# Kernel tuning notes

Measured on AMD Instinct MI355X. Metric: run time of the kernel, lower is better.

The kernel has to match this reference:

```python
import jax, jax.numpy as jnp
import numpy as np

B, N, D, H = 1, 512, 128, 128  # batch, seq, pair dim, hidden dim
EPS = 1e-6  # flax nnx LayerNorm default epsilon


def _layernorm(x, scale, bias):
    m = jnp.mean(x, axis=-1, keepdims=True)
    v = jnp.var(x, axis=-1, keepdims=True)
    return (x - m) * jax.lax.rsqrt(v + EPS) * scale + bias


def setup_inputs() -> dict:
    key = jax.random.key(0)
    ks = jax.random.split(key, 12)
    s = 0.02  # param init scale
    inp = {
        "x": jax.random.normal(ks[0], (B, N, N, D), jnp.float32),
        "src_mask": jnp.ones((B, N), jnp.float32),
        # first LayerNorm
        "ln1_scale": jnp.ones((D,), jnp.float32),
        "ln1_bias": jnp.zeros((D,), jnp.float32),
        # left/right projections
        "wl": jax.random.normal(ks[1], (D, H), jnp.float32) * s,
        "bl": jnp.zeros((H,), jnp.float32),
        "wr": jax.random.normal(ks[2], (D, H), jnp.float32) * s,
        "br": jnp.zeros((H,), jnp.float32),
        # gates (original inits kernel=0, bias=1; use small random kernels + bias=1 for a nontrivial baseline)
        "wlg": jax.random.normal(ks[3], (D, H), jnp.float32) * s,
        "blg": jnp.ones((H,), jnp.float32),
        "wrg": jax.random.normal(ks[4], (D, H), jnp.float32) * s,
        "brg": jnp.ones((H,), jnp.float32),
        "wog": jax.random.normal(ks[5], (D, H), jnp.float32) * s,
        "bog": jnp.ones((H,), jnp.float32),
        # output LayerNorm + projection
        "ln2_scale": jnp.ones((H,), jnp.float32),
        "ln2_bias": jnp.zeros((H,), jnp.float32),
        "wo": jax.random.normal(ks[6], (H, D), jnp.float32) * s,
        "bo": jnp.zeros((D,), jnp.float32),
    }
    return inp


def reference(x, src_mask, ln1_scale, ln1_bias, wl, bl, wr, br, wlg, blg,
              wrg, brg, wog, bog, ln2_scale, ln2_bias, wo, bo):
    # mask[b,i,j] = src_mask[b,i] * src_mask[b,j]  -> [B,N,N,1]
    sm = src_mask.astype(jnp.float32)
    mask = (sm[:, :, None] * sm[:, None, :])[..., None]

    xn = _layernorm(x, ln1_scale, ln1_bias)  # [B,N,N,D]

    # projections, mask, gates (gating after transpose in the original is
    # elementwise, hence equivalent applied pre-transpose)
    left = (xn @ wl + bl) * mask * jax.nn.sigmoid(xn @ wlg + blg)   # [B,N,N,H]
    right = (xn @ wr + br) * mask * jax.nn.sigmoid(xn @ wrg + brg)  # [B,N,N,H]
    out_gate = jax.nn.sigmoid(xn @ wog + bog)                       # [B,N,N,H]

    # 'ingoing' mix: out[b,i,j,d] = sum_k left[b,k,i,d] * right[b,k,j,d]
    out = jnp.einsum('bkid,bkjd->bijd', left, right)

    out = _layernorm(out, ln2_scale, ln2_bias) * out_gate
    return out @ wo + bo
```

## Files before the change

kernel.cpp:

```cpp
#include <hip/hip_runtime.h>
#include <hip/hip_bf16.h>


#define NSEQ 512
#define NN 262144
#define PL 262400
#define DMODEL 128

typedef __attribute__((ext_vector_type(8))) short short8;
typedef __attribute__((ext_vector_type(4))) float f32x4;

__device__ __forceinline__ unsigned short f2b(float f) {
    __hip_bfloat16 h = __float2bfloat16(f);
    return *reinterpret_cast<unsigned short*>(&h);
}
__device__ __forceinline__ float b2f(unsigned short u) {
    __hip_bfloat16 h;
    *reinterpret_cast<unsigned short*>(&h) = u;
    return __bfloat162float(h);
}
__device__ __forceinline__ unsigned int cvt_pk_bf16(float lo, float hi) {
    unsigned int r;
    asm("v_cvt_pk_bf16_f32 %0, %1, %2" : "=v"(r) : "v"(lo), "v"(hi));
    return r;
}
__device__ __forceinline__ float sigfast(float x) {
    return __builtin_amdgcn_rcpf(1.f + __builtin_amdgcn_exp2f(x * -1.44269504f));
}

__global__ __launch_bounds__(256) void k_wt_all(
    const float* __restrict__ w0, const float* __restrict__ w1,
    const float* __restrict__ w2, const float* __restrict__ w3,
    const float* __restrict__ w4, const float* __restrict__ w5,
    unsigned short* __restrict__ wt) {
    int bid = blockIdx.x;
    int mat = bid >> 6;
    const float* w = (mat == 0) ? w0 : (mat == 1) ? w1 : (mat == 2) ? w2
                   : (mat == 3) ? w3 : (mat == 4) ? w4 : w5;
    int idx = (bid & 63) * 256 + threadIdx.x;
    int d = idx >> 7, h = idx & 127;
    wt[mat * 16384 + h * 128 + d] = f2b(w[idx]);
}

__global__ __launch_bounds__(256) void k_ln1(const float* __restrict__ x,
                                             const float* __restrict__ sc,
                                             const float* __restrict__ bi,
                                             unsigned short* __restrict__ xn) {
    int t = threadIdx.x;
    int l = t & 31;
    size_t row = (size_t)blockIdx.x * 8 + (t >> 5);
    float4 v = *(const float4*)(x + row * DMODEL + l * 4);
    float s  = v.x + v.y + v.z + v.w;
    float sq = v.x * v.x + v.y * v.y + v.z * v.z + v.w * v.w;
    #pragma unroll
    for (int m = 1; m < 32; m <<= 1) {
        s  += __shfl_xor(s, m);
        sq += __shfl_xor(sq, m);
    }
    float mean = s * (1.f / 128.f);
    float var  = sq * (1.f / 128.f) - mean * mean;
    float inv  = rsqrtf(var + 1e-6f);
    float4 scv = *(const float4*)(sc + l * 4);
    float4 biv = *(const float4*)(bi + l * 4);
    uint2 pk;
    pk.x = cvt_pk_bf16((v.x - mean) * inv * scv.x + biv.x,
                       (v.y - mean) * inv * scv.y + biv.y);
    pk.y = cvt_pk_bf16((v.z - mean) * inv * scv.z + biv.z,
                       (v.w - mean) * inv * scv.w + biv.w);
    *(uint2*)(xn + row * DMODEL + l * 4) = pk;
}

__global__ __launch_bounds__(256, 2) void k_proj(
    const unsigned short* __restrict__ xn,
    const float* __restrict__ src_mask,
    const unsigned short* __restrict__ wt,
    const float* __restrict__ bl,  const float* __restrict__ blg,
    const float* __restrict__ br,  const float* __restrict__ brg,
    const float* __restrict__ bog,
    unsigned short* __restrict__ left_t,
    unsigned short* __restrict__ right_t,
    unsigned short* __restrict__ og) {
    __shared__ __align__(16) unsigned short As[64 * 136];
    const int t = threadIdx.x;
    const int lane = t & 63;
    const int wv = t >> 6;
    const int a0 = blockIdx.x * 64;
    const int b  = blockIdx.y;
    const int n0 = wv * 32;

    short8 bfA[2][4], bfB[2][4];
    auto loadB = [&](short8 (&dst)[2][4], int mat) {
        const unsigned short* base = wt + mat * 16384 + (lane >> 4) * 8;
        #pragma unroll
        for (int nf = 0; nf < 2; ++nf)
            #pragma unroll
            for (int kc = 0; kc < 4; ++kc)
                dst[nf][kc] = *(const short8*)(
                    base + (n0 + nf * 16 + (lane & 15)) * 128 + kc * 32);
    };
    loadB(bfA, 0);
    loadB(bfB, 1);

    #pragma unroll
    for (int it = 0; it < 4; ++it) {
        int idx = it * 256 + t;
        int row = idx >> 4, c = idx & 15;
        *(short8*)(&As[row * 136 + c * 8]) =
            *(const short8*)(xn + ((size_t)(a0 + row) * NSEQ + b) * DMODEL + c * 8);
    }
    __syncthreads();

    short8 af[4][4];
    #pragma unroll
    for (int mf = 0; mf < 4; ++mf)
        #pragma unroll
        for (int kc = 0; kc < 4; ++kc)
            af[mf][kc] = *(const short8*)(
                &As[(mf * 16 + (lane & 15)) * 136 + kc * 32 + (lane >> 4) * 8]);

    f32x4 acc0[4][2], acc1[4][2];
    float smb = src_mask[b];

    auto mmat = [&](f32x4 (&acc)[4][2], short8 (&bf)[2][4]) {
        #pragma unroll
        for (int mf = 0; mf < 4; ++mf)
            #pragma unroll
            for (int nf = 0; nf < 2; ++nf)
                acc[mf][nf] = f32x4{0.f, 0.f, 0.f, 0.f};
        #pragma unroll
        for (int kc = 0; kc < 4; ++kc)
            #pragma unroll
            for (int mf = 0; mf < 4; ++mf)
                #pragma unroll
                for (int nf = 0; nf < 2; ++nf)
                    acc[mf][nf] = __builtin_amdgcn_mfma_f32_16x16x32_bf16(
                        af[mf][kc], bf[nf][kc], acc[mf][nf], 0, 0, 0);
    };
    auto epi_pair = [&](const float* b1, const float* b2, unsigned short* dst) {
        float mkv[16];
        #pragma unroll
        for (int mf = 0; mf < 4; ++mf)
            #pragma unroll
            for (int j = 0; j < 4; ++j)
                mkv[mf * 4 + j] =
                    src_mask[a0 + mf * 16 + ((lane >> 4) << 2) + j] * smb;
        #pragma unroll
        for (int nf = 0; nf < 2; ++nf) {
            int h = n0 + nf * 16 + (lane & 15);
            float b1v = b1[h], b2v = b2[h];
            #pragma unroll
            for (int mf = 0; mf < 4; ++mf) {
                int abase = a0 + mf * 16 + ((lane >> 4) << 2);
                float o_[4];
                #pragma unroll
                for (int j = 0; j < 4; ++j) {
                    float pv = acc0[mf][nf][j] + b1v;
                    float gv = acc1[mf][nf][j] + b2v;
                    o_[j] = pv * mkv[mf * 4 + j] * sigfast(gv);
                }
                uint2 pk;
                pk.x = cvt_pk_bf16(o_[0], o_[1]);
                pk.y = cvt_pk_bf16(o_[2], o_[3]);
                *(uint2*)(dst + (size_t)h * PL + (size_t)b * NSEQ + abase) = pk;
            }
        }
    };

    mmat(acc0, bfA);
    loadB(bfA, 2);
    mmat(acc1, bfB);
    loadB(bfB, 3);
    epi_pair(bl, blg, left_t);
    mmat(acc0, bfA);
    loadB(bfA, 4);
    mmat(acc1, bfB);
    epi_pair(br, brg, right_t);
    mmat(acc0, bfA);

    __syncthreads();
    #pragma unroll
    for (int nf = 0; nf < 2; ++nf) {
        int h = n0 + nf * 16 + (lane & 15);
        float bv = bog[h];
        #pragma unroll
        for (int mf = 0; mf < 4; ++mf) {
            int rloc = mf * 16 + ((lane >> 4) << 2);
            #pragma unroll
            for (int j = 0; j < 4; ++j)
                As[(rloc + j) * 136 + h] = f2b(sigfast(acc0[mf][nf][j] + bv));
        }
    }
    __syncthreads();
    #pragma unroll
    for (int it = 0; it < 4; ++it) {
        int idx = it * 256 + t;
        int row = idx >> 4, c = idx & 15;
        *(short8*)(og + ((size_t)(a0 + row) * NSEQ + b) * DMODEL + c * 8) =
            *(const short8*)(&As[row * 136 + c * 8]);
    }
}

__global__ __launch_bounds__(256) void k_einsum(
    const unsigned short* __restrict__ lt,
    const unsigned short* __restrict__ rt,
    unsigned short* __restrict__ mid) {
    __shared__ __align__(16) unsigned short As[2][128 * 36];
    __shared__ __align__(16) unsigned short Bs[2][128 * 36];
    const int t = threadIdx.x, lane = t & 63, wv = t >> 6;
    const int bid = blockIdx.x;
    const int xcd = bid & 7, slot = bid >> 3;
    const int d = xcd * 16 + (slot >> 4);
    const int tile = slot & 15;
    const int i0 = (tile >> 2) * 128, j0 = (tile & 3) * 128;
    const int m0 = (wv >> 1) * 64, n0 = (wv & 1) * 64;
    const unsigned short* Ag = lt + (size_t)d * PL;
    const unsigned short* Bg = rt + (size_t)d * PL;

    const int row0 = t >> 2, sub0 = t & 3;
    const int row1 = (256 + t) >> 2, sub1 = t & 3;

    short8 ra[2], rb[2];
    auto loadTile = [&](int k0) {
        ra[0] = *(const short8*)(Ag + (size_t)(i0 + row0) * NSEQ + k0 + sub0 * 8);
        rb[0] = *(const short8*)(Bg + (size_t)(j0 + row0) * NSEQ + k0 + sub0 * 8);
        ra[1] = *(const short8*)(Ag + (size_t)(i0 + row1) * NSEQ + k0 + sub1 * 8);
        rb[1] = *(const short8*)(Bg + (size_t)(j0 + row1) * NSEQ + k0 + sub1 * 8);
    };
    auto writeTile = [&](int buf) {
        *(short8*)(&As[buf][row0 * 36 + sub0 * 8]) = ra[0];
        *(short8*)(&Bs[buf][row0 * 36 + sub0 * 8]) = rb[0];
        *(short8*)(&As[buf][row1 * 36 + sub1 * 8]) = ra[1];
        *(short8*)(&Bs[buf][row1 * 36 + sub1 * 8]) = rb[1];
    };

    f32x4 acc[4][4];
    #pragma unroll
    for (int mf = 0; mf < 4; ++mf)
        #pragma unroll
        for (int nf = 0; nf < 4; ++nf)
            acc[mf][nf] = f32x4{0.f, 0.f, 0.f, 0.f};

    loadTile(0);
    writeTile(0);
    int cur = 0;
    const int ko = (lane >> 4) * 8;
    for (int it = 0; it < 16; ++it) {
        __syncthreads();
        if (it < 15) loadTile((it + 1) * 32);
        short8 af[4], bf[4];
        #pragma unroll
        for (int mf = 0; mf < 4; ++mf)
            af[mf] = *(const short8*)(&As[cur][(m0 + mf * 16 + (lane & 15)) * 36 + ko]);
        #pragma unroll
        for (int nf = 0; nf < 4; ++nf)
            bf[nf] = *(const short8*)(&Bs[cur][(n0 + nf * 16 + (lane & 15)) * 36 + ko]);
        #pragma unroll
        for (int mf = 0; mf < 4; ++mf)
            #pragma unroll
            for (int nf = 0; nf < 4; ++nf)
                acc[mf][nf] = __builtin_amdgcn_mfma_f32_16x16x32_bf16(
                    af[mf], bf[nf], acc[mf][nf], 0, 0, 0);
        if (it < 15) writeTile(cur ^ 1);
        cur ^= 1;
    }
    unsigned short* out = mid + (size_t)d * PL;
    #pragma unroll
    for (int mf = 0; mf < 4; ++mf) {
        int rbase = i0 + m0 + mf * 16 + ((lane >> 4) << 2);
        #pragma unroll
        for (int nf = 0; nf < 4; ++nf) {
            int col = j0 + n0 + nf * 16 + (lane & 15);
            #pragma unroll
            for (int j = 0; j < 4; ++j)
                out[(size_t)(rbase + j) * NSEQ + col] = f2b(acc[mf][nf][j]);
        }
    }
}

__global__ __launch_bounds__(128) void k_ln2gate(
    const unsigned short* __restrict__ mid,
    const unsigned short* __restrict__ og,
    const float* __restrict__ sc, const float* __restrict__ bi,
    unsigned short* __restrict__ g) {
    __shared__ __align__(16) unsigned short lo[128 * 136];
    const int t = threadIdx.x;
    const size_t p0 = (size_t)blockIdx.x * 128;
    const size_t p = p0 + t;

    unsigned int vals[64];
    float s = 0.f, sq = 0.f;
    #pragma unroll
    for (int d2 = 0; d2 < 64; ++d2) {
        unsigned int a = mid[(size_t)(2 * d2)     * PL + p];
        unsigned int c = mid[(size_t)(2 * d2 + 1) * PL + p];
        vals[d2] = a | (c << 16);
        float fa = b2f((unsigned short)a), fc = b2f((unsigned short)c);
        s += fa + fc; sq += fa * fa + fc * fc;
    }
    float mean = s * (1.f / 128.f);
    float var  = sq * (1.f / 128.f) - mean * mean;
    float inv  = rsqrtf(var + 1e-6f);
    #pragma unroll
    for (int c = 0; c < 16; ++c) {
        short8 ov = *(const short8*)(og + p * DMODEL + c * 8);
        float y[8];
        #pragma unroll
        for (int e = 0; e < 8; ++e) {
            int d = c * 8 + e;
            unsigned int w = vals[d >> 1];
            float v = b2f((unsigned short)((d & 1) ? (w >> 16) : (w & 0xffff)));
            y[e] = ((v - mean) * inv * sc[d] + bi[d]) * b2f((unsigned short)ov[e]);
        }
        uint4 pk;
        pk.x = cvt_pk_bf16(y[0], y[1]);
        pk.y = cvt_pk_bf16(y[2], y[3]);
        pk.z = cvt_pk_bf16(y[4], y[5]);
        pk.w = cvt_pk_bf16(y[6], y[7]);
        *(uint4*)(&lo[t * 136 + c * 8]) = pk;
    }
    __syncthreads();
    #pragma unroll
    for (int i = 0; i < 16; ++i) {
        int idx = i * 128 + t;
        int row = idx >> 4, ch = idx & 15;
        *(short8*)(g + (p0 + row) * DMODEL + ch * 8) =
            *(const short8*)(&lo[row * 136 + ch * 8]);
    }
}

__global__ __launch_bounds__(256) void k_out(
    const unsigned short* __restrict__ g,
    const unsigned short* __restrict__ wt_o,
    const float* __restrict__ bo,
    float* __restrict__ out) {
    __shared__ __align__(16) unsigned short As[64 * 136];
    __shared__ __align__(16) unsigned short Bs[128 * 136];
    const int t = threadIdx.x, lane = t & 63, wv = t >> 6;
    const size_t r0 = (size_t)blockIdx.x * 64;
    const int n0 = wv * 32;
    for (int it = 0; it < 4; ++it) {
        int idx = it * 256 + t;
        int row = idx >> 4, c = idx & 15;
        *(short8*)(&As[row * 136 + c * 8]) =
            *(const short8*)(g + (r0 + row) * DMODEL + c * 8);
    }
    for (int it = 0; it < 8; ++it) {
        int idx = it * 256 + t;
        int h = idx >> 4, c = idx & 15;
        *(short8*)(&Bs[h * 136 + c * 8]) = *(const short8*)(wt_o + h * 128 + c * 8);
    }
    __syncthreads();
    f32x4 acc[4][2];
    #pragma unroll
    for (int mf = 0; mf < 4; ++mf)
        #pragma unroll
        for (int nf = 0; nf < 2; ++nf)
            acc[mf][nf] = f32x4{0.f, 0.f, 0.f, 0.f};
    #pragma unroll
    for (int kc = 0; kc < 4; ++kc) {
        int ko = kc * 32 + (lane >> 4) * 8;
        short8 af[4], bf[2];
        #pragma unroll
        for (int mf = 0; mf < 4; ++mf)
            af[mf] = *(const short8*)(&As[(mf * 16 + (lane & 15)) * 136 + ko]);
        #pragma unroll
        for (int nf = 0; nf < 2; ++nf)
            bf[nf] = *(const short8*)(&Bs[(n0 + nf * 16 + (lane & 15)) * 136 + ko]);
        #pragma unroll
        for (int mf = 0; mf < 4; ++mf)
            #pragma unroll
            for (int nf = 0; nf < 2; ++nf)
                acc[mf][nf] = __builtin_amdgcn_mfma_f32_16x16x32_bf16(
                    af[mf], bf[nf], acc[mf][nf], 0, 0, 0);
    }
    #pragma unroll
    for (int nf = 0; nf < 2; ++nf) {
        int n = n0 + nf * 16 + (lane & 15);
        float bv = bo[n];
        #pragma unroll
        for (int mf = 0; mf < 4; ++mf) {
            int rb = mf * 16 + ((lane >> 4) << 2);
            #pragma unroll
            for (int j = 0; j < 4; ++j)
                out[(r0 + rb + j) * DMODEL + n] = acc[mf][nf][j] + bv;
        }
    }
}

extern "C" void kernel_launch(void* const* d_in, const int* in_sizes, int n_in,
                              void* d_out, int out_size, void* d_ws, size_t ws_size,
                              hipStream_t stream) {
    const float* x    = (const float*)d_in[0];
    const float* sm   = (const float*)d_in[1];
    const float* ln1s = (const float*)d_in[2];
    const float* ln1b = (const float*)d_in[3];
    const float* wl   = (const float*)d_in[4];
    const float* bl   = (const float*)d_in[5];
    const float* wr   = (const float*)d_in[6];
    const float* br   = (const float*)d_in[7];
    const float* wlg  = (const float*)d_in[8];
    const float* blg  = (const float*)d_in[9];
    const float* wrg  = (const float*)d_in[10];
    const float* brg  = (const float*)d_in[11];
    const float* wog  = (const float*)d_in[12];
    const float* bog  = (const float*)d_in[13];
    const float* ln2s = (const float*)d_in[14];
    const float* ln2b = (const float*)d_in[15];
    const float* wo   = (const float*)d_in[16];
    const float* bo   = (const float*)d_in[17];
    float* out = (float*)d_out;

    char* ws = (char*)d_ws;
    const size_t SZ_XN = 67108864ull;
    const size_t SZ_PL = (size_t)PL * 128 * 2;
    unsigned short* wt  = (unsigned short*)ws;
    unsigned short* xn  = (unsigned short*)(ws + 196608);
    unsigned short* lt  = (unsigned short*)(ws + 196608 + SZ_XN);
    unsigned short* rt  = (unsigned short*)(ws + 196608 + SZ_XN + SZ_PL);
    unsigned short* ogb = (unsigned short*)(ws + 196608 + SZ_XN + 2 * SZ_PL);
    unsigned short* mid = (unsigned short*)(ws + 196608 + 2 * SZ_XN + 2 * SZ_PL);
    unsigned short* gb  = xn;

    k_wt_all<<<384, 256, 0, stream>>>(wl, wlg, wr, wrg, wog, wo, wt);
    k_ln1<<<32768, 256, 0, stream>>>(x, ln1s, ln1b, xn);
    k_proj<<<dim3(8, 512), 256, 0, stream>>>(xn, sm, wt,
                                             bl, blg, br, brg, bog, lt, rt, ogb);
    k_einsum<<<2048, 256, 0, stream>>>(lt, rt, mid);
    k_ln2gate<<<2048, 128, 0, stream>>>(mid, ogb, ln2s, ln2b, gb);
    k_out<<<4096, 256, 0, stream>>>(gb, wt + 5 * 16384, bo, out);
}
```

Baseline: 324.7 us.

## Fuse LN2-gate into output projection and stage einsum tiles via direct global-to-LDS loads

```diff
diff --git a/kernel.cpp b/kernel.cpp
--- a/kernel.cpp
+++ b/kernel.cpp
@@ -26,6 +26,11 @@
 }
 __device__ __forceinline__ float sigfast(float x) {
     return __builtin_amdgcn_rcpf(1.f + __builtin_amdgcn_exp2f(x * -1.44269504f));
+}
+__device__ __forceinline__ void gload_lds16(const void* g, void* l) {
+    __builtin_amdgcn_global_load_lds(
+        (const __attribute__((address_space(1))) void*)g,
+        (__attribute__((address_space(3))) void*)l, 16, 0, 0);
 }
 
 __global__ __launch_bounds__(256) void k_wt_all(
@@ -204,8 +209,8 @@
     const unsigned short* __restrict__ lt,
     const unsigned short* __restrict__ rt,
     unsigned short* __restrict__ mid) {
-    __shared__ __align__(16) unsigned short As[2][128 * 36];
-    __shared__ __align__(16) unsigned short Bs[2][128 * 36];
+    __shared__ __align__(16) unsigned short As[2][128 * 32];
+    __shared__ __align__(16) unsigned short Bs[2][128 * 32];
     const int t = threadIdx.x, lane = t & 63, wv = t >> 6;
     const int bid = blockIdx.x;
     const int xcd = bid & 7, slot = bid >> 3;
@@ -216,21 +221,16 @@
     const unsigned short* Ag = lt + (size_t)d * PL;
     const unsigned short* Bg = rt + (size_t)d * PL;
 
-    const int row0 = t >> 2, sub0 = t & 3;
-    const int row1 = (256 + t) >> 2, sub1 = t & 3;
-
-    short8 ra[2], rb[2];
-    auto loadTile = [&](int k0) {
-        ra[0] = *(const short8*)(Ag + (size_t)(i0 + row0) * NSEQ + k0 + sub0 * 8);
-        rb[0] = *(const short8*)(Bg + (size_t)(j0 + row0) * NSEQ + k0 + sub0 * 8);
-        ra[1] = *(const short8*)(Ag + (size_t)(i0 + row1) * NSEQ + k0 + sub1 * 8);
-        rb[1] = *(const short8*)(Bg + (size_t)(j0 + row1) * NSEQ + k0 + sub1 * 8);
-    };
-    auto writeTile = [&](int buf) {
-        *(short8*)(&As[buf][row0 * 36 + sub0 * 8]) = ra[0];
-        *(short8*)(&Bs[buf][row0 * 36 + sub0 * 8]) = rb[0];
-        *(short8*)(&As[buf][row1 * 36 + sub1 * 8]) = ra[1];
-        *(short8*)(&Bs[buf][row1 * 36 + sub1 * 8]) = rb[1];
+    auto stage = [&](int buf, int k0) {
+        #pragma unroll
+        for (int r = 0; r < 2; ++r) {
+            int c = r * 256 + wv * 64 + lane;
+            int row = c >> 2, sub = c & 3;
+            gload_lds16(Ag + (size_t)(i0 + row) * NSEQ + k0 + sub * 8,
+                        &As[buf][(r * 256 + wv * 64) * 8]);
+            gload_lds16(Bg + (size_t)(j0 + row) * NSEQ + k0 + sub * 8,
+                        &Bs[buf][(r * 256 + wv * 64) * 8]);
+        }
     };
 
     f32x4 acc[4][4];
@@ -240,27 +240,25 @@
         for (int nf = 0; nf < 4; ++nf)
             acc[mf][nf] = f32x4{0.f, 0.f, 0.f, 0.f};
 
-    loadTile(0);
-    writeTile(0);
+    stage(0, 0);
     int cur = 0;
     const int ko = (lane >> 4) * 8;
     for (int it = 0; it < 16; ++it) {
         __syncthreads();
-        if (it < 15) loadTile((it + 1) * 32);
+        if (it < 15) stage(cur ^ 1, (it + 1) * 32);
         short8 af[4], bf[4];
         #pragma unroll
         for (int mf = 0; mf < 4; ++mf)
-            af[mf] = *(const short8*)(&As[cur][(m0 + mf * 16 + (lane & 15)) * 36 + ko]);
+            af[mf] = *(const short8*)(&As[cur][(m0 + mf * 16 + (lane & 15)) * 32 + ko]);
         #pragma unroll
         for (int nf = 0; nf < 4; ++nf)
-            bf[nf] = *(const short8*)(&Bs[cur][(n0 + nf * 16 + (lane & 15)) * 36 + ko]);
+            bf[nf] = *(const short8*)(&Bs[cur][(n0 + nf * 16 + (lane & 15)) * 32 + ko]);
         #pragma unroll
         for (int mf = 0; mf < 4; ++mf)
             #pragma unroll
             for (int nf = 0; nf < 4; ++nf)
                 acc[mf][nf] = __builtin_amdgcn_mfma_f32_16x16x32_bf16(
                     af[mf], bf[nf], acc[mf][nf], 0, 0, 0);
-        if (it < 15) writeTile(cur ^ 1);
         cur ^= 1;
     }
     unsigned short* out = mid + (size_t)d * PL;
@@ -277,79 +275,65 @@
     }
 }
 
-__global__ __launch_bounds__(128) void k_ln2gate(
+__global__ __launch_bounds__(256) void k_lnout(
     const unsigned short* __restrict__ mid,
     const unsigned short* __restrict__ og,
     const float* __restrict__ sc, const float* __restrict__ bi,
-    unsigned short* __restrict__ g) {
-    __shared__ __align__(16) unsigned short lo[128 * 136];
-    const int t = threadIdx.x;
-    const size_t p0 = (size_t)blockIdx.x * 128;
-    const size_t p = p0 + t;
-
-    unsigned int vals[64];
+    const unsigned short* __restrict__ wt_o,
+    const float* __restrict__ bo,
+    float* __restrict__ out) {
+    __shared__ __align__(16) unsigned short As[64 * 136];
+    __shared__ __align__(16) unsigned short Bs[128 * 136];
+    __shared__ float2 st[4][64];
+    const int t = threadIdx.x, lane = t & 63, wv = t >> 6;
+    const size_t p0 = (size_t)blockIdx.x * 64;
+    const size_t p = p0 + lane;
+    const int d0 = wv * 32;
+
+    #pragma unroll
+    for (int it = 0; it < 8; ++it) {
+        int idx = it * 256 + t;
+        int h = idx >> 4, c = idx & 15;
+        *(short8*)(&Bs[h * 136 + c * 8]) = *(const short8*)(wt_o + h * 128 + c * 8);
+    }
+
+    unsigned short v16[32];
     float s = 0.f, sq = 0.f;
     #pragma unroll
-    for (int d2 = 0; d2 < 64; ++d2) {
-        unsigned int a = mid[(size_t)(2 * d2)     * PL + p];
-        unsigned int c = mid[(size_t)(2 * d2 + 1) * PL + p];
-        vals[d2] = a | (c << 16);
-        float fa = b2f((unsigned short)a), fc = b2f((unsigned short)c);
-        s += fa + fc; sq += fa * fa + fc * fc;
-    }
-    float mean = s * (1.f / 128.f);
-    float var  = sq * (1.f / 128.f) - mean * mean;
-    float inv  = rsqrtf(var + 1e-6f);
-    #pragma unroll
-    for (int c = 0; c < 16; ++c) {
-        short8 ov = *(const short8*)(og + p * DMODEL + c * 8);
+    for (int e = 0; e < 32; ++e) {
+        unsigned short u = mid[(size_t)(d0 + e) * PL + p];
+        v16[e] = u;
+        float f = b2f(u);
+        s += f; sq += f * f;
+    }
+    st[wv][lane] = float2{s, sq};
+    __syncthreads();
+    float2 s0 = st[0][lane], s1 = st[1][lane], s2 = st[2][lane], s3 = st[3][lane];
+    float S = s0.x + s1.x + s2.x + s3.x;
+    float Q = s0.y + s1.y + s2.y + s3.y;
+    float mean = S * (1.f / 128.f);
+    float inv  = rsqrtf(Q * (1.f / 128.f) - mean * mean + 1e-6f);
+
+    #pragma unroll
+    for (int c = 0; c < 4; ++c) {
+        short8 ov = *(const short8*)(og + p * DMODEL + d0 + c * 8);
         float y[8];
         #pragma unroll
         for (int e = 0; e < 8; ++e) {
-            int d = c * 8 + e;
-            unsigned int w = vals[d >> 1];
-            float v = b2f((unsigned short)((d & 1) ? (w >> 16) : (w & 0xffff)));
-            y[e] = ((v - mean) * inv * sc[d] + bi[d]) * b2f((unsigned short)ov[e]);
+            int dd = d0 + c * 8 + e;
+            float v = b2f(v16[c * 8 + e]);
+            y[e] = ((v - mean) * inv * sc[dd] + bi[dd]) * b2f((unsigned short)ov[e]);
         }
         uint4 pk;
         pk.x = cvt_pk_bf16(y[0], y[1]);
         pk.y = cvt_pk_bf16(y[2], y[3]);
         pk.z = cvt_pk_bf16(y[4], y[5]);
         pk.w = cvt_pk_bf16(y[6], y[7]);
-        *(uint4*)(&lo[t * 136 + c * 8]) = pk;
+        *(uint4*)(&As[lane * 136 + d0 + c * 8]) = pk;
     }
     __syncthreads();
-    #pragma unroll
-    for (int i = 0; i < 16; ++i) {
-        int idx = i * 128 + t;
-        int row = idx >> 4, ch = idx & 15;
-        *(short8*)(g + (p0 + row) * DMODEL + ch * 8) =
-            *(const short8*)(&lo[row * 136 + ch * 8]);
-    }
-}
-
-__global__ __launch_bounds__(256) void k_out(
-    const unsigned short* __restrict__ g,
-    const unsigned short* __restrict__ wt_o,
-    const float* __restrict__ bo,
-    float* __restrict__ out) {
-    __shared__ __align__(16) unsigned short As[64 * 136];
-    __shared__ __align__(16) unsigned short Bs[128 * 136];
-    const int t = threadIdx.x, lane = t & 63, wv = t >> 6;
-    const size_t r0 = (size_t)blockIdx.x * 64;
+
     const int n0 = wv * 32;
-    for (int it = 0; it < 4; ++it) {
-        int idx = it * 256 + t;
-        int row = idx >> 4, c = idx & 15;
-        *(short8*)(&As[row * 136 + c * 8]) =
-            *(const short8*)(g + (r0 + row) * DMODEL + c * 8);
-    }
-    for (int it = 0; it < 8; ++it) {
-        int idx = it * 256 + t;
-        int h = idx >> 4, c = idx & 15;
-        *(short8*)(&Bs[h * 136 + c * 8]) = *(const short8*)(wt_o + h * 128 + c * 8);
-    }
-    __syncthreads();
     f32x4 acc[4][2];
     #pragma unroll
     for (int mf = 0; mf < 4; ++mf)
@@ -382,7 +366,7 @@
             int rb = mf * 16 + ((lane >> 4) << 2);
             #pragma unroll
             for (int j = 0; j < 4; ++j)
-                out[(r0 + rb + j) * DMODEL + n] = acc[mf][nf][j] + bv;
+                out[(p0 + rb + j) * DMODEL + n] = acc[mf][nf][j] + bv;
         }
     }
 }
@@ -419,13 +403,12 @@
     unsigned short* rt  = (unsigned short*)(ws + 196608 + SZ_XN + SZ_PL);
     unsigned short* ogb = (unsigned short*)(ws + 196608 + SZ_XN + 2 * SZ_PL);
     unsigned short* mid = (unsigned short*)(ws + 196608 + 2 * SZ_XN + 2 * SZ_PL);
-    unsigned short* gb  = xn;
 
     k_wt_all<<<384, 256, 0, stream>>>(wl, wlg, wr, wrg, wog, wo, wt);
     k_ln1<<<32768, 256, 0, stream>>>(x, ln1s, ln1b, xn);
     k_proj<<<dim3(8, 512), 256, 0, stream>>>(xn, sm, wt,
                                              bl, blg, br, brg, bog, lt, rt, ogb);
     k_einsum<<<2048, 256, 0, stream>>>(lt, rt, mid);
-    k_ln2gate<<<2048, 128, 0, stream>>>(mid, ogb, ln2s, ln2b, gb);
-    k_out<<<4096, 256, 0, stream>>>(gb, wt + 5 * 16384, bo, out);
-}
+    k_lnout<<<4096, 256, 0, stream>>>(mid, ogb, ln2s, ln2b,
+                                      wt + 5 * 16384, bo, out);
+}
```

Result: faster. 295.8 us, median of 4 (-8.9%).
